# Performance work log

Hardware: AMD Instinct MI355X
Metric: run time of the kernel (lower is better)

Reference implementation:

```python
import jax, jax.numpy as jnp
import numpy as np

B, IN, H = 8192, 1024, 1024

def _ln(x, g, b, eps=1e-5):
    mu = jnp.mean(x, axis=-1, keepdims=True)
    var = jnp.mean(jnp.square(x - mu), axis=-1, keepdims=True)
    return (x - mu) * jax.lax.rsqrt(var + eps) * g + b

def setup_inputs() -> dict:
    key = jax.random.key(0)
    ks = jax.random.split(key, 8)
    s_h = 1.0 / np.sqrt(H)
    s_i = 1.0 / np.sqrt(IN)
    inp = {
        'x': jax.random.normal(ks[0], (B, IN), jnp.float32),
        'h': jax.random.normal(ks[1], (B, H), jnp.float32),
        'W_r': jax.random.uniform(ks[2], (H, H), jnp.float32, -s_h, s_h),
        'U_r': jax.random.uniform(ks[3], (H, IN), jnp.float32, -s_i, s_i),
        'W_u': jax.random.uniform(ks[4], (H, H), jnp.float32, -s_h, s_h),
        'U_u': jax.random.uniform(ks[5], (H, IN), jnp.float32, -s_i, s_i),
        'W_c': jax.random.uniform(ks[6], (H, H), jnp.float32, -s_h, s_h),
        'U_c': jax.random.uniform(ks[7], (H, IN), jnp.float32, -s_i, s_i),
        # LayerNorm params: rows = [r_hidden, r_input, u_hidden, u_input, c_hidden, c_input]
        'ln_gamma': 0.1 * jnp.ones((6, H), jnp.float32),
        'ln_beta': jnp.zeros((6, H), jnp.float32),
    }
    return inp

def reference(x, h, W_r, U_r, W_u, U_u, W_c, U_c, ln_gamma, ln_beta):
    g, b = ln_gamma, ln_beta
    # nn.Linear(bias=False): y = x @ W.T
    r = jax.nn.sigmoid(_ln(h @ W_r.T, g[0], b[0]) + _ln(x @ U_r.T, g[1], b[1]))
    u = jax.nn.sigmoid(_ln(h @ W_u.T, g[2], b[2]) + _ln(x @ U_u.T, g[3], b[3]))
    c = jnp.tanh(_ln((h * r) @ W_c.T, g[4], b[4]) + _ln(x @ U_c.T, g[5], b[5]))
    return (1.0 - u) * h + u * c
```

## Files before the change

kernel.cpp:

```cpp
#include <hip/hip_runtime.h>
#include <cstdint>
#include <cstddef>

typedef unsigned short u16;
typedef unsigned char u8;
typedef __attribute__((ext_vector_type(8))) short bf16x8;
typedef __attribute__((ext_vector_type(4))) float f32x4;
typedef __attribute__((ext_vector_type(4))) int i32x4;
typedef __attribute__((ext_vector_type(8))) int i32x8;

__device__ inline float bf2f(u16 u) { return __uint_as_float(((unsigned)u) << 16); }
__device__ inline unsigned f2bf(float f) {
  unsigned u = __float_as_uint(f);
  u += 0x7fffu + ((u >> 16) & 1u);
  return u >> 16;
}

__device__ inline unsigned f2fp8(float f) {
  unsigned s = (__float_as_uint(f) >> 31) << 7;
  float a = fabsf(f);
  if (a >= 0.015625f) {
    unsigned u = __float_as_uint(a);
    u += 0x7FFFFu + ((u >> 20) & 1u);
    unsigned e = (u >> 23) - 120u;
    unsigned m = (u >> 20) & 7u;
    return s | (e << 3) | m;
  }
  int m = (int)rintf(a * 512.0f);
  return s | (unsigned)m;
}

__device__ inline void async16(const void* g, void* l) {
  __builtin_amdgcn_global_load_lds(
      (const __attribute__((address_space(1))) void*)g,
      (__attribute__((address_space(3))) void*)l, 16, 0, 0);
}

__device__ inline i32x8 join8(i32x4 lo, i32x4 hi) {
  i32x8 r;
  r[0] = lo[0]; r[1] = lo[1]; r[2] = lo[2]; r[3] = lo[3];
  r[4] = hi[0]; r[5] = hi[1]; r[6] = hi[2]; r[7] = hi[3];
  return r;
}

__device__ inline void unpack8(uint4 q, float* o) {
  o[0] = bf2f((u16)(q.x & 0xffffu)); o[1] = bf2f((u16)(q.x >> 16));
  o[2] = bf2f((u16)(q.y & 0xffffu)); o[3] = bf2f((u16)(q.y >> 16));
  o[4] = bf2f((u16)(q.z & 0xffffu)); o[5] = bf2f((u16)(q.z >> 16));
  o[6] = bf2f((u16)(q.w & 0xffffu)); o[7] = bf2f((u16)(q.w >> 16));
}

__device__ inline uint4 pack8(const float* v) {
  uint4 q;
  q.x = f2bf(v[0]) | (f2bf(v[1]) << 16);
  q.y = f2bf(v[2]) | (f2bf(v[3]) << 16);
  q.z = f2bf(v[4]) | (f2bf(v[5]) << 16);
  q.w = f2bf(v[6]) | (f2bf(v[7]) << 16);
  return q;
}

__device__ inline float fast_sigmoid(float z) {
  return 1.0f / (1.0f + exp2f(-1.4426950408889634f * z));
}
__device__ inline float fast_tanh(float z) {
  return 1.0f - 2.0f / (1.0f + exp2f(2.8853900817779268f * z));
}

struct ConvArgs2 {
  const float* x; const float* h; const float* wr; const float* ur;
  const float* wbf[4];
  u16* xb; u16* hb; u8* x8; u8* h8; u8* w8r; u8* w8u;
  u16* wbo[4];
};

__global__ __launch_bounds__(256) void convert_all(ConvArgs2 a) {
  const int b = blockIdx.x;
  const int t = threadIdx.x;
  if (b < 16384) {
    const bool isx = b < 8192;
    const int off = isx ? b : b - 8192;
    const float* __restrict__ s = isx ? a.x : a.h;
    u16* __restrict__ db = isx ? a.xb : a.hb;
    u8*  __restrict__ d8 = isx ? a.x8 : a.h8;
    const int i = (off * 256 + t) * 4;
    float4 v = *(const float4*)(s + i);
    uint2 o;
    o.x = f2bf(v.x) | (f2bf(v.y) << 16);
    o.y = f2bf(v.z) | (f2bf(v.w) << 16);
    *(uint2*)(db + i) = o;
    unsigned q = f2fp8(v.x) | (f2fp8(v.y) << 8) | (f2fp8(v.z) << 16) | (f2fp8(v.w) << 24);
    *(unsigned*)(d8 + i) = q;
  } else if (b < 18432) {
    const bool isr = b < 17408;
    const int off = isr ? b - 16384 : b - 17408;
    const float* __restrict__ s = isr ? a.wr : a.ur;
    u8* __restrict__ d8 = isr ? a.w8r : a.w8u;
    const int i = (off * 256 + t) * 4;
    float4 v = *(const float4*)(s + i);
    unsigned q = f2fp8(v.x * 8192.f) | (f2fp8(v.y * 8192.f) << 8) |
                 (f2fp8(v.z * 8192.f) << 16) | (f2fp8(v.w * 8192.f) << 24);
    *(unsigned*)(d8 + i) = q;
  } else {
    const int tt = b - 18432;
    const int which = tt >> 10;
    const int off = tt & 1023;
    const float* __restrict__ s = a.wbf[which];
    u16* __restrict__ d = a.wbo[which];
    const int i = (off * 256 + t) * 4;
    float4 v = *(const float4*)(s + i);
    uint2 o;
    o.x = f2bf(v.x) | (f2bf(v.y) << 16);
    o.y = f2bf(v.z) | (f2bf(v.w) << 16);
    *(uint2*)(d + i) = o;
  }
}

struct GemmF8 { const u8* A[2]; const u8* Bw[2]; u16* Y[2]; };

__global__ __launch_bounds__(512, 2) void gemm_fp8(GemmF8 args) {
  const int p = blockIdx.x;
  const int wg = (p & 7) * 32 + (p >> 3);
  const int gate = wg >> 7;
  const int rem  = wg & 127;
  const int rblk = rem >> 2;
  const int cblk = rem & 3;

  const u8* __restrict__ A  = args.A[gate];
  const u8* __restrict__ Bw = args.Bw[gate];
  u16* __restrict__ Y = args.Y[gate];

  __shared__ __attribute__((aligned(16))) u8 sm[2][2][2][128 * 128];

  const int tid  = threadIdx.x;
  const int lane = tid & 63;
  const int w    = tid >> 6;
  const int wm   = w >> 2;
  const int wn   = w & 3;

  const int l8   = lane >> 3;
  const int sgrp = (lane & 7) ^ l8;
  const u8* aSrc = A  + ((size_t)(rblk * 256 + w * 8 + l8) << 10) + sgrp * 16;
  const u8* bSrc = Bw + ((size_t)(cblk * 256 + w * 8 + l8) << 10) + sgrp * 16;
  const int ldsW = w * 8 * 128;

  const int sw = lane & 7;
  const int g0 = (lane >> 4) * 2;
  const int o0 = ((g0 ^ sw) << 4);
  const int o1 = (((g0 + 1) ^ sw) << 4);
  const int frR = (lane & 15) * 128;

  f32x4 acc_lo[4][4] = {};
  f32x4 acc_hi[4][4] = {};

  auto stage = [&](const u8* src, int tt, int op, int half) {
    const int d = tt & 1;
    const u8* s = src + (size_t)half * 131072 + tt * 128;
    u8* l0 = &sm[d][op][half][ldsW];
    async16(s, l0);
    async16(s + 65536, l0 + 8192);
  };

  stage(bSrc, 0, 1, 0); stage(bSrc, 0, 1, 1);
  stage(aSrc, 0, 0, 0); stage(aSrc, 0, 0, 1);
  stage(bSrc, 1, 1, 0); stage(bSrc, 1, 1, 1);
  stage(aSrc, 1, 0, 0);
  asm volatile("s_waitcnt vmcnt(6)" ::: "memory");
  __builtin_amdgcn_s_barrier();

  for (int t = 0; t < 8; ++t) {
    const int d = t & 1;
    const u8* baseA = &sm[d][0][wm][0];
    const u8* baseB = &sm[d][1][wn >> 1][(wn & 1) * 8192];

    i32x8 alo[4], bfg[4];
#pragma unroll
    for (int m = 0; m < 4; ++m) {
      const int ra = frR + m * 2048;
      alo[m] = join8(*(const i32x4*)&baseA[ra + o0], *(const i32x4*)&baseA[ra + o1]);
    }
#pragma unroll
    for (int n = 0; n < 4; ++n) {
      const int rbb = frR + n * 2048;
      bfg[n] = join8(*(const i32x4*)&baseB[rbb + o0], *(const i32x4*)&baseB[rbb + o1]);
    }
    if (t + 1 < 8) stage(aSrc, t + 1, 0, 1);
    __builtin_amdgcn_s_barrier();
    asm volatile("s_waitcnt lgkmcnt(0)" ::: "memory");
    __builtin_amdgcn_s_setprio(1);
#pragma unroll
    for (int m = 0; m < 4; ++m)
#pragma unroll
      for (int n = 0; n < 2; ++n)
        acc_lo[m][n] = __builtin_amdgcn_mfma_scale_f32_16x16x128_f8f6f4(
            alo[m], bfg[n], acc_lo[m][n], 0, 0, 0, 127, 0, 114);
    __builtin_amdgcn_s_setprio(0);
    __builtin_amdgcn_s_barrier();

    if (t + 2 < 8) stage(bSrc, t + 2, 1, 0);
    __builtin_amdgcn_s_barrier();
    __builtin_amdgcn_s_setprio(1);
#pragma unroll
    for (int m = 0; m < 4; ++m)
#pragma unroll
      for (int n = 2; n < 4; ++n)
        acc_lo[m][n] = __builtin_amdgcn_mfma_scale_f32_16x16x128_f8f6f4(
            alo[m], bfg[n], acc_lo[m][n], 0, 0, 0, 127, 0, 114);
    __builtin_amdgcn_s_setprio(0);
    __builtin_amdgcn_s_barrier();

    i32x8 ahi[4];
#pragma unroll
    for (int m = 0; m < 4; ++m) {
      const int ra = frR + m * 2048 + 8192;
      ahi[m] = join8(*(const i32x4*)&baseA[ra + o0], *(const i32x4*)&baseA[ra + o1]);
    }
    if (t + 2 < 8) stage(bSrc, t + 2, 1, 1);
    __builtin_amdgcn_s_barrier();
    asm volatile("s_waitcnt lgkmcnt(0)" ::: "memory");
    __builtin_amdgcn_s_setprio(1);
#pragma unroll
    for (int m = 0; m < 4; ++m)
#pragma unroll
      for (int n = 0; n < 2; ++n)
        acc_hi[m][n] = __builtin_amdgcn_mfma_scale_f32_16x16x128_f8f6f4(
            ahi[m], bfg[n], acc_hi[m][n], 0, 0, 0, 127, 0, 114);
    __builtin_amdgcn_s_setprio(0);
    __builtin_amdgcn_s_barrier();

    if (t + 2 < 8) stage(aSrc, t + 2, 0, 0);
    __builtin_amdgcn_s_barrier();
    __builtin_amdgcn_s_setprio(1);
#pragma unroll
    for (int m = 0; m < 4; ++m)
#pragma unroll
      for (int n = 2; n < 4; ++n)
        acc_hi[m][n] = __builtin_amdgcn_mfma_scale_f32_16x16x128_f8f6f4(
            ahi[m], bfg[n], acc_hi[m][n], 0, 0, 0, 127, 0, 114);
    __builtin_amdgcn_s_setprio(0);
    if (t < 6) asm volatile("s_waitcnt vmcnt(6)" ::: "memory");
    else       asm volatile("s_waitcnt vmcnt(0)" ::: "memory");
    __builtin_amdgcn_s_barrier();
  }

  const int rBase = rblk * 256 + wm * 128 + (lane >> 4) * 4;
  const int cBase = cblk * 256 + wn * 64 + (lane & 15);
#pragma unroll
  for (int m = 0; m < 4; ++m) {
#pragma unroll
    for (int i = 0; i < 4; ++i) {
      const size_t r0 = (size_t)(rBase + m * 16 + i) * 1024 + cBase;
#pragma unroll
      for (int n = 0; n < 4; ++n) {
        Y[r0 + n * 16]             = (u16)f2bf(acc_lo[m][n][i]);
        Y[r0 + 64 * 1024 + n * 16] = (u16)f2bf(acc_hi[m][n][i]);
      }
    }
  }
}

struct Gemm4 { const u16* A[4]; const u16* Bw[4]; u16* Y[4]; };

__global__ __launch_bounds__(512, 2) void gemm_8ph(Gemm4 args) {
  const int p = blockIdx.x;
  const int wg = (p & 7) * 64 + (p >> 3);
  const int gate = wg >> 7;
  const int rem  = wg & 127;
  const int rblk = rem >> 2;
  const int cblk = rem & 3;

  const u16* __restrict__ A  = args.A[gate];
  const u16* __restrict__ Bw = args.Bw[gate];
  u16* __restrict__ Y = args.Y[gate];

  __shared__ __attribute__((aligned(16))) u16 sm[2][2][2][128 * 64];

  const int tid  = threadIdx.x;
  const int lane = tid & 63;
  const int w    = tid >> 6;
  const int wm   = w >> 2;
  const int wn   = w & 3;

  const int l8   = lane >> 3;
  const int sgrp = (lane & 7) ^ l8;
  const u16* aSrc = A  + ((size_t)(rblk * 256 + w * 8 + l8) << 10) + sgrp * 8;
  const u16* bSrc = Bw + ((size_t)(cblk * 256 + w * 8 + l8) << 10) + sgrp * 8;
  const int ldsW = w * 8 * 64;

  const int fr = (lane & 15) * 64 + ((((lane >> 4) ^ (lane & 7))) << 3);

  f32x4 acc_lo[4][4] = {};
  f32x4 acc_hi[4][4] = {};

  auto stage = [&](const u16* src, int tt, int op, int half) {
    const int d = tt & 1;
    const u16* s = src + (size_t)half * 131072 + tt * 64;
    u16* l0 = &sm[d][op][half][ldsW];
    async16(s, l0);
    async16(s + 65536, l0 + 4096);
  };

  stage(bSrc, 0, 1, 0); stage(bSrc, 0, 1, 1);
  stage(aSrc, 0, 0, 0); stage(aSrc, 0, 0, 1);
  stage(bSrc, 1, 1, 0); stage(bSrc, 1, 1, 1);
  stage(aSrc, 1, 0, 0);
  asm volatile("s_waitcnt vmcnt(6)" ::: "memory");
  __builtin_amdgcn_s_barrier();

  for (int t = 0; t < 16; ++t) {
    const int d = t & 1;
    const u16* baseA = &sm[d][0][wm][0];
    const u16* baseB = &sm[d][1][wn >> 1][(wn & 1) * 4096];

    bf16x8 alo[2][4], bfg[2][4];
#pragma unroll
    for (int kk = 0; kk < 2; ++kk) {
      const int fo = fr ^ (kk << 5);
#pragma unroll
      for (int m = 0; m < 4; ++m) alo[kk][m] = *(const bf16x8*)(baseA + m * 1024 + fo);
#pragma unroll
      for (int n = 0; n < 4; ++n) bfg[kk][n] = *(const bf16x8*)(baseB + n * 1024 + fo);
    }
    if (t + 1 < 16) stage(aSrc, t + 1, 0, 1);
    __builtin_amdgcn_s_barrier();
    asm volatile("s_waitcnt lgkmcnt(0)" ::: "memory");
    __builtin_amdgcn_s_setprio(1);
#pragma unroll
    for (int m = 0; m < 4; ++m)
#pragma unroll
      for (int n = 0; n < 2; ++n)
#pragma unroll
        for (int kk = 0; kk < 2; ++kk)
          acc_lo[m][n] = __builtin_amdgcn_mfma_f32_16x16x32_bf16(alo[kk][m], bfg[kk][n], acc_lo[m][n], 0, 0, 0);
    __builtin_amdgcn_s_setprio(0);
    __builtin_amdgcn_s_barrier();

    if (t + 2 < 16) stage(bSrc, t + 2, 1, 0);
    __builtin_amdgcn_s_barrier();
    __builtin_amdgcn_s_setprio(1);
#pragma unroll
    for (int m = 0; m < 4; ++m)
#pragma unroll
      for (int n = 2; n < 4; ++n)
#pragma unroll
        for (int kk = 0; kk < 2; ++kk)
          acc_lo[m][n] = __builtin_amdgcn_mfma_f32_16x16x32_bf16(alo[kk][m], bfg[kk][n], acc_lo[m][n], 0, 0, 0);
    __builtin_amdgcn_s_setprio(0);
    __builtin_amdgcn_s_barrier();

    bf16x8 ahi[2][4];
#pragma unroll
    for (int kk = 0; kk < 2; ++kk) {
      const int fo = fr ^ (kk << 5);
#pragma unroll
      for (int m = 0; m < 4; ++m) ahi[kk][m] = *(const bf16x8*)(baseA + (m + 4) * 1024 + fo);
    }
    if (t + 2 < 16) stage(bSrc, t + 2, 1, 1);
    __builtin_amdgcn_s_barrier();
    asm volatile("s_waitcnt lgkmcnt(0)" ::: "memory");
    __builtin_amdgcn_s_setprio(1);
#pragma unroll
    for (int m = 0; m < 4; ++m)
#pragma unroll
      for (int n = 0; n < 2; ++n)
#pragma unroll
        for (int kk = 0; kk < 2; ++kk)
          acc_hi[m][n] = __builtin_amdgcn_mfma_f32_16x16x32_bf16(ahi[kk][m], bfg[kk][n], acc_hi[m][n], 0, 0, 0);
    __builtin_amdgcn_s_setprio(0);
    __builtin_amdgcn_s_barrier();

    if (t + 2 < 16) stage(aSrc, t + 2, 0, 0);
    __builtin_amdgcn_s_barrier();
    __builtin_amdgcn_s_setprio(1);
#pragma unroll
    for (int m = 0; m < 4; ++m)
#pragma unroll
      for (int n = 2; n < 4; ++n)
#pragma unroll
        for (int kk = 0; kk < 2; ++kk)
          acc_hi[m][n] = __builtin_amdgcn_mfma_f32_16x16x32_bf16(ahi[kk][m], bfg[kk][n], acc_hi[m][n], 0, 0, 0);
    __builtin_amdgcn_s_setprio(0);
    if (t < 14) asm volatile("s_waitcnt vmcnt(6)" ::: "memory");
    else        asm volatile("s_waitcnt vmcnt(0)" ::: "memory");
    __builtin_amdgcn_s_barrier();
  }

  const int rBase = rblk * 256 + wm * 128 + (lane >> 4) * 4;
  const int cBase = cblk * 256 + wn * 64 + (lane & 15);
#pragma unroll
  for (int m = 0; m < 4; ++m) {
#pragma unroll
    for (int i = 0; i < 4; ++i) {
      const size_t r0 = (size_t)(rBase + m * 16 + i) * 1024 + cBase;
#pragma unroll
      for (int n = 0; n < 4; ++n) {
        Y[r0 + n * 16]             = (u16)f2bf(acc_lo[m][n][i]);
        Y[r0 + 64 * 1024 + n * 16] = (u16)f2bf(acc_hi[m][n][i]);
      }
    }
  }
}

__global__ __launch_bounds__(256) void rgate_kernel(
    const u16* __restrict__ Yrh, const u16* __restrict__ Yrx,
    const u16* __restrict__ hb, const float* __restrict__ gamma,
    const float* __restrict__ beta, u16* __restrict__ hrb) {
  const int row  = blockIdx.x * 4 + (threadIdx.x >> 6);
  const int lane = threadIdx.x & 63;
  const size_t rb = (size_t)row * 1024;

  uint4 qa[2], qb[2], qh[2];
  qa[0] = *(const uint4*)(Yrh + rb + lane * 8);
  qa[1] = *(const uint4*)(Yrh + rb + 512 + lane * 8);
  qb[0] = *(const uint4*)(Yrx + rb + lane * 8);
  qb[1] = *(const uint4*)(Yrx + rb + 512 + lane * 8);
  qh[0] = *(const uint4*)(hb  + rb + lane * 8);
  qh[1] = *(const uint4*)(hb  + rb + 512 + lane * 8);

  float s0 = 0.f, s0q = 0.f, s1 = 0.f, s1q = 0.f;
  float tmp[8];
#pragma unroll
  for (int c = 0; c < 2; c++) {
    unpack8(qa[c], tmp);
#pragma unroll
    for (int j = 0; j < 8; j++) { s0 += tmp[j]; s0q += tmp[j] * tmp[j]; }
    unpack8(qb[c], tmp);
#pragma unroll
    for (int j = 0; j < 8; j++) { s1 += tmp[j]; s1q += tmp[j] * tmp[j]; }
  }
#pragma unroll
  for (int off = 1; off < 64; off <<= 1) {
    s0 += __shfl_xor(s0, off, 64);  s0q += __shfl_xor(s0q, off, 64);
    s1 += __shfl_xor(s1, off, 64);  s1q += __shfl_xor(s1q, off, 64);
  }

  const float inv = 1.0f / 1024.0f;
  const float mu0 = s0 * inv, rs0 = rsqrtf(s0q * inv - mu0 * mu0 + 1e-5f);
  const float mu1 = s1 * inv, rs1 = rsqrtf(s1q * inv - mu1 * mu1 + 1e-5f);

#pragma unroll
  for (int c = 0; c < 2; c++) {
    const int cb = c * 512 + lane * 8;
    float va[8], vb[8], vh[8], o[8];
    unpack8(qa[c], va); unpack8(qb[c], vb); unpack8(qh[c], vh);
#pragma unroll
    for (int j = 0; j < 8; j++) {
      const float ln0 = (va[j] - mu0) * rs0 * gamma[cb + j] + beta[cb + j];
      const float ln1 = (vb[j] - mu1) * rs1 * gamma[1024 + cb + j] + beta[1024 + cb + j];
      const float rg = fast_sigmoid(ln0 + ln1);
      o[j] = vh[j] * rg;
    }
    *(uint4*)(hrb + rb + cb) = pack8(o);
  }
}

__global__ __launch_bounds__(256) void final_fuse(
    const u16* __restrict__ Yuh, const u16* __restrict__ Yux,
    const u16* __restrict__ Ych, const u16* __restrict__ Ycx,
    const float* __restrict__ h, const float* __restrict__ gamma,
    const float* __restrict__ beta, float* __restrict__ out) {
  const int row  = blockIdx.x * 4 + (threadIdx.x >> 6);
  const int lane = threadIdx.x & 63;
  const size_t rb = (size_t)row * 1024;

  uint4 q0[2], q1[2], q2[2], q3[2];
  float4 hf[4];
#pragma unroll
  for (int c = 0; c < 2; c++) {
    const int cb = c * 512 + lane * 8;
    q0[c] = *(const uint4*)(Yuh + rb + cb);
    q1[c] = *(const uint4*)(Yux + rb + cb);
    q2[c] = *(const uint4*)(Ych + rb + cb);
    q3[c] = *(const uint4*)(Ycx + rb + cb);
    hf[c * 2]     = *(const float4*)(h + rb + cb);
    hf[c * 2 + 1] = *(const float4*)(h + rb + cb + 4);
  }

  float s[8] = {0.f, 0.f, 0.f, 0.f, 0.f, 0.f, 0.f, 0.f};
  float tmp[8];
#pragma unroll
  for (int c = 0; c < 2; c++) {
    unpack8(q0[c], tmp);
#pragma unroll
    for (int j = 0; j < 8; j++) { s[0] += tmp[j]; s[1] += tmp[j] * tmp[j]; }
    unpack8(q1[c], tmp);
#pragma unroll
    for (int j = 0; j < 8; j++) { s[2] += tmp[j]; s[3] += tmp[j] * tmp[j]; }
    unpack8(q2[c], tmp);
#pragma unroll
    for (int j = 0; j < 8; j++) { s[4] += tmp[j]; s[5] += tmp[j] * tmp[j]; }
    unpack8(q3[c], tmp);
#pragma unroll
    for (int j = 0; j < 8; j++) { s[6] += tmp[j]; s[7] += tmp[j] * tmp[j]; }
  }
#pragma unroll
  for (int off = 1; off < 64; off <<= 1) {
#pragma unroll
    for (int q = 0; q < 8; q++) s[q] += __shfl_xor(s[q], off, 64);
  }

  const float inv = 1.0f / 1024.0f;
  const float mu0 = s[0] * inv, rs0 = rsqrtf(s[1] * inv - mu0 * mu0 + 1e-5f);
  const float mu1 = s[2] * inv, rs1 = rsqrtf(s[3] * inv - mu1 * mu1 + 1e-5f);
  const float mu2 = s[4] * inv, rs2 = rsqrtf(s[5] * inv - mu2 * mu2 + 1e-5f);
  const float mu3 = s[6] * inv, rs3 = rsqrtf(s[7] * inv - mu3 * mu3 + 1e-5f);

#pragma unroll
  for (int c = 0; c < 2; c++) {
    const int cb = c * 512 + lane * 8;
    float v0[8], v1[8], v2[8], v3[8];
    unpack8(q0[c], v0); unpack8(q1[c], v1); unpack8(q2[c], v2); unpack8(q3[c], v3);
    const float* hv = (const float*)&hf[c * 2];
    float o[8];
#pragma unroll
    for (int j = 0; j < 8; j++) {
      const int cc = cb + j;
      const float ln2 = (v0[j] - mu0) * rs0 * gamma[2 * 1024 + cc] + beta[2 * 1024 + cc];
      const float ln3 = (v1[j] - mu1) * rs1 * gamma[3 * 1024 + cc] + beta[3 * 1024 + cc];
      const float ln4 = (v2[j] - mu2) * rs2 * gamma[4 * 1024 + cc] + beta[4 * 1024 + cc];
      const float ln5 = (v3[j] - mu3) * rs3 * gamma[5 * 1024 + cc] + beta[5 * 1024 + cc];
      const float u  = fast_sigmoid(ln2 + ln3);
      const float cg = fast_tanh(ln4 + ln5);
      o[j] = (1.0f - u) * hv[j] + u * cg;
    }
    *(float4*)(out + rb + cb)     = *(float4*)&o[0];
    *(float4*)(out + rb + cb + 4) = *(float4*)&o[4];
  }
}

extern "C" void kernel_launch(void* const* d_in, const int* in_sizes, int n_in,
                              void* d_out, int out_size, void* d_ws, size_t ws_size,
                              hipStream_t stream) {
  const float* x  = (const float*)d_in[0];
  const float* h  = (const float*)d_in[1];
  const float* W_r = (const float*)d_in[2];
  const float* U_r = (const float*)d_in[3];
  const float* W_u = (const float*)d_in[4];
  const float* U_u = (const float*)d_in[5];
  const float* W_c = (const float*)d_in[6];
  const float* U_c = (const float*)d_in[7];
  const float* gamma = (const float*)d_in[8];
  const float* beta  = (const float*)d_in[9];
  float* out = (float*)d_out;

  char* ws = (char*)d_ws;
  const size_t MB = 1024 * 1024;
  const size_t SZ_ACT = 16 * MB;

  u16* xb = (u16*)(ws);
  u16* hb = (u16*)(ws + 16 * MB);
  u16* wb[4];
  for (int i = 0; i < 4; i++) wb[i] = (u16*)(ws + (32 + 2 * i) * MB);
  u8* w8r = (u8*)(ws + 40 * MB);
  u8* w8u = (u8*)(ws + 41 * MB);
  char* ybase = ws + 42 * MB;
  u16* Y0 = (u16*)(ybase);
  u16* Y1 = (u16*)(ybase + SZ_ACT);
  u16* Y2 = (u16*)(ybase + 2 * SZ_ACT);
  u16* Y3 = (u16*)(ybase + 3 * SZ_ACT);
  u16* Y5 = (u16*)(ybase + 4 * SZ_ACT);
  u8* x8 = (u8*)Y5;
  u8* h8 = (u8*)Y5 + 8 * MB;

  ConvArgs2 ca = {};
  ca.x = x; ca.h = h; ca.wr = W_r; ca.ur = U_r;
  ca.wbf[0] = W_u; ca.wbf[1] = U_u; ca.wbf[2] = W_c; ca.wbf[3] = U_c;
  ca.xb = xb; ca.hb = hb; ca.x8 = x8; ca.h8 = h8; ca.w8r = w8r; ca.w8u = w8u;
  ca.wbo[0] = (u16*)(ws + 32 * MB); ca.wbo[1] = (u16*)(ws + 34 * MB);
  ca.wbo[2] = (u16*)(ws + 36 * MB); ca.wbo[3] = (u16*)(ws + 38 * MB);
  convert_all<<<22528, 256, 0, stream>>>(ca);

  GemmF8 gf = {};
  gf.A[0] = h8; gf.Bw[0] = w8r; gf.Y[0] = Y0;
  gf.A[1] = x8; gf.Bw[1] = w8u; gf.Y[1] = Y1;
  gemm_fp8<<<256, 512, 0, stream>>>(gf);

  rgate_kernel<<<2048, 256, 0, stream>>>(Y0, Y1, hb, gamma, beta, Y1);

  Gemm4 gb = {};
  gb.A[0] = xb; gb.Bw[0] = wb[1]; gb.Y[0] = Y3;
  gb.A[1] = xb; gb.Bw[1] = wb[3]; gb.Y[1] = Y5;
  gb.A[2] = hb; gb.Bw[2] = wb[0]; gb.Y[2] = Y2;
  gb.A[3] = Y1; gb.Bw[3] = wb[2]; gb.Y[3] = Y0;
  gemm_8ph<<<512, 512, 0, stream>>>(gb);

  final_fuse<<<2048, 256, 0, stream>>>(Y2, Y3, Y0, Y5, h, gamma, beta, out);
}
```

Baseline: 270.4 us.

## Prefetch next-tile LDS fragments at loop tail and pin schedule with sched barriers

Both GEMM kernels (fp8 scaled MFMA and bf16 MFMA) now load the A-lo and B fragments for the next K step from the other LDS buffer at the end of each iteration. Those loads overlap the barrier and the start of the next iteration instead of stalling before the first MFMA block. The first MFMA block waits on lgkmcnt(4) and the later blocks on lgkmcnt(0), so the loads are retired in stages. Scheduling barriers stop the compiler from moving instructions across these phases, at the cost of extra live registers and fewer chances for it to reorder.

```diff
diff --git a/kernel.cpp b/kernel.cpp
--- a/kernel.cpp
+++ b/kernel.cpp
@@ -65,6 +65,8 @@
 __device__ inline float fast_tanh(float z) {
   return 1.0f - 2.0f / (1.0f + exp2f(2.8853900817779268f * z));
 }
+
+#define SB0() __builtin_amdgcn_sched_barrier(0)
 
 struct ConvArgs2 {
   const float* x; const float* h; const float* wr; const float* ur;
@@ -167,12 +169,10 @@
   asm volatile("s_waitcnt vmcnt(6)" ::: "memory");
   __builtin_amdgcn_s_barrier();
 
-  for (int t = 0; t < 8; ++t) {
-    const int d = t & 1;
-    const u8* baseA = &sm[d][0][wm][0];
-    const u8* baseB = &sm[d][1][wn >> 1][(wn & 1) * 8192];
-
-    i32x8 alo[4], bfg[4];
+  i32x8 alo[4], bfg[4], ahi[4];
+  {
+    const u8* baseA = &sm[0][0][wm][0];
+    const u8* baseB = &sm[0][1][wn >> 1][(wn & 1) * 8192];
 #pragma unroll
     for (int m = 0; m < 4; ++m) {
       const int ra = frR + m * 2048;
@@ -183,9 +183,20 @@
       const int rbb = frR + n * 2048;
       bfg[n] = join8(*(const i32x4*)&baseB[rbb + o0], *(const i32x4*)&baseB[rbb + o1]);
     }
+  }
+  SB0();
+
+  for (int t = 0; t < 8; ++t) {
+    const int d = t & 1;
+    const u8* baseA  = &sm[d][0][wm][0];
+    const u8* baseA2 = &sm[d ^ 1][0][wm][0];
+    const u8* baseB2 = &sm[d ^ 1][1][wn >> 1][(wn & 1) * 8192];
+
     if (t + 1 < 8) stage(aSrc, t + 1, 0, 1);
-    __builtin_amdgcn_s_barrier();
-    asm volatile("s_waitcnt lgkmcnt(0)" ::: "memory");
+    SB0();
+    __builtin_amdgcn_s_barrier();
+    asm volatile("s_waitcnt lgkmcnt(4)" ::: "memory");
+    SB0();
     __builtin_amdgcn_s_setprio(1);
 #pragma unroll
     for (int m = 0; m < 4; ++m)
@@ -194,10 +205,14 @@
         acc_lo[m][n] = __builtin_amdgcn_mfma_scale_f32_16x16x128_f8f6f4(
             alo[m], bfg[n], acc_lo[m][n], 0, 0, 0, 127, 0, 114);
     __builtin_amdgcn_s_setprio(0);
+    SB0();
     __builtin_amdgcn_s_barrier();
 
     if (t + 2 < 8) stage(bSrc, t + 2, 1, 0);
-    __builtin_amdgcn_s_barrier();
+    SB0();
+    __builtin_amdgcn_s_barrier();
+    asm volatile("s_waitcnt lgkmcnt(0)" ::: "memory");
+    SB0();
     __builtin_amdgcn_s_setprio(1);
 #pragma unroll
     for (int m = 0; m < 4; ++m)
@@ -206,17 +221,20 @@
         acc_lo[m][n] = __builtin_amdgcn_mfma_scale_f32_16x16x128_f8f6f4(
             alo[m], bfg[n], acc_lo[m][n], 0, 0, 0, 127, 0, 114);
     __builtin_amdgcn_s_setprio(0);
-    __builtin_amdgcn_s_barrier();
-
-    i32x8 ahi[4];
+    SB0();
 #pragma unroll
     for (int m = 0; m < 4; ++m) {
       const int ra = frR + m * 2048 + 8192;
       ahi[m] = join8(*(const i32x4*)&baseA[ra + o0], *(const i32x4*)&baseA[ra + o1]);
     }
+    SB0();
+    __builtin_amdgcn_s_barrier();
+
     if (t + 2 < 8) stage(bSrc, t + 2, 1, 1);
+    SB0();
     __builtin_amdgcn_s_barrier();
     asm volatile("s_waitcnt lgkmcnt(0)" ::: "memory");
+    SB0();
     __builtin_amdgcn_s_setprio(1);
 #pragma unroll
     for (int m = 0; m < 4; ++m)
@@ -225,9 +243,11 @@
         acc_hi[m][n] = __builtin_amdgcn_mfma_scale_f32_16x16x128_f8f6f4(
             ahi[m], bfg[n], acc_hi[m][n], 0, 0, 0, 127, 0, 114);
     __builtin_amdgcn_s_setprio(0);
+    SB0();
     __builtin_amdgcn_s_barrier();
 
     if (t + 2 < 8) stage(aSrc, t + 2, 0, 0);
+    SB0();
     __builtin_amdgcn_s_barrier();
     __builtin_amdgcn_s_setprio(1);
 #pragma unroll
@@ -237,8 +257,23 @@
         acc_hi[m][n] = __builtin_amdgcn_mfma_scale_f32_16x16x128_f8f6f4(
             ahi[m], bfg[n], acc_hi[m][n], 0, 0, 0, 127, 0, 114);
     __builtin_amdgcn_s_setprio(0);
+    SB0();
     if (t < 6) asm volatile("s_waitcnt vmcnt(6)" ::: "memory");
     else       asm volatile("s_waitcnt vmcnt(0)" ::: "memory");
+    SB0();
+    if (t + 1 < 8) {
+#pragma unroll
+      for (int m = 0; m < 4; ++m) {
+        const int ra = frR + m * 2048;
+        alo[m] = join8(*(const i32x4*)&baseA2[ra + o0], *(const i32x4*)&baseA2[ra + o1]);
+      }
+#pragma unroll
+      for (int n = 0; n < 4; ++n) {
+        const int rbb = frR + n * 2048;
+        bfg[n] = join8(*(const i32x4*)&baseB2[rbb + o0], *(const i32x4*)&baseB2[rbb + o1]);
+      }
+    }
+    SB0();
     __builtin_amdgcn_s_barrier();
   }
 
@@ -306,57 +341,76 @@
   asm volatile("s_waitcnt vmcnt(6)" ::: "memory");
   __builtin_amdgcn_s_barrier();
 
+  bf16x8 alo[2][4], bfg[2][4], ahi[2][4];
+  {
+    const u16* baseA = &sm[0][0][wm][0];
+    const u16* baseB = &sm[0][1][wn >> 1][(wn & 1) * 4096];
+#pragma unroll
+    for (int kk = 0; kk < 2; ++kk) {
+      const int fo = fr ^ (kk << 5);
+#pragma unroll
+      for (int m = 0; m < 4; ++m) alo[kk][m] = *(const bf16x8*)(baseA + m * 1024 + fo);
+    }
+#pragma unroll
+    for (int n = 0; n < 4; ++n)
+#pragma unroll
+      for (int kk = 0; kk < 2; ++kk)
+        bfg[kk][n] = *(const bf16x8*)(baseB + n * 1024 + (fr ^ (kk << 5)));
+  }
+  SB0();
+
   for (int t = 0; t < 16; ++t) {
     const int d = t & 1;
-    const u16* baseA = &sm[d][0][wm][0];
-    const u16* baseB = &sm[d][1][wn >> 1][(wn & 1) * 4096];
-
-    bf16x8 alo[2][4], bfg[2][4];
+    const u16* baseA  = &sm[d][0][wm][0];
+    const u16* baseA2 = &sm[d ^ 1][0][wm][0];
+    const u16* baseB2 = &sm[d ^ 1][1][wn >> 1][(wn & 1) * 4096];
+
+    if (t + 1 < 16) stage(aSrc, t + 1, 0, 1);
+    SB0();
+    __builtin_amdgcn_s_barrier();
+    asm volatile("s_waitcnt lgkmcnt(4)" ::: "memory");
+    SB0();
+    __builtin_amdgcn_s_setprio(1);
+#pragma unroll
+    for (int m = 0; m < 4; ++m)
+#pragma unroll
+      for (int n = 0; n < 2; ++n)
+#pragma unroll
+        for (int kk = 0; kk < 2; ++kk)
+          acc_lo[m][n] = __builtin_amdgcn_mfma_f32_16x16x32_bf16(alo[kk][m], bfg[kk][n], acc_lo[m][n], 0, 0, 0);
+    __builtin_amdgcn_s_setprio(0);
+    SB0();
+    __builtin_amdgcn_s_barrier();
+
+    if (t + 2 < 16) stage(bSrc, t + 2, 1, 0);
+    SB0();
+    __builtin_amdgcn_s_barrier();
+    asm volatile("s_waitcnt lgkmcnt(0)" ::: "memory");
+    SB0();
+    __builtin_amdgcn_s_setprio(1);
+#pragma unroll
+    for (int m = 0; m < 4; ++m)
+#pragma unroll
+      for (int n = 2; n < 4; ++n)
+#pragma unroll
+        for (int kk = 0; kk < 2; ++kk)
+          acc_lo[m][n] = __builtin_amdgcn_mfma_f32_16x16x32_bf16(alo[kk][m], bfg[kk][n], acc_lo[m][n], 0, 0, 0);
+    __builtin_amdgcn_s_setprio(0);
+    SB0();
 #pragma unroll
     for (int kk = 0; kk < 2; ++kk) {
       const int fo = fr ^ (kk << 5);
 #pragma unroll
-      for (int m = 0; m < 4; ++m) alo[kk][m] = *(const bf16x8*)(baseA + m * 1024 + fo);
-#pragma unroll
-      for (int n = 0; n < 4; ++n) bfg[kk][n] = *(const bf16x8*)(baseB + n * 1024 + fo);
-    }
-    if (t + 1 < 16) stage(aSrc, t + 1, 0, 1);
+      for (int m = 0; m < 4; ++m) ahi[kk][m] = *(const bf16x8*)(baseA + (m + 4) * 1024 + fo);
+    }
+    SB0();
+    __builtin_amdgcn_s_barrier();
+
+    if (t + 2 < 16) stage(bSrc, t + 2, 1, 1);
+    SB0();
     __builtin_amdgcn_s_barrier();
     asm volatile("s_waitcnt lgkmcnt(0)" ::: "memory");
-    __builtin_amdgcn_s_setprio(1);
-#pragma unroll
-    for (int m = 0; m < 4; ++m)
-#pragma unroll
-      for (int n = 0; n < 2; ++n)
-#pragma unroll
-        for (int kk = 0; kk < 2; ++kk)
-          acc_lo[m][n] = __builtin_amdgcn_mfma_f32_16x16x32_bf16(alo[kk][m], bfg[kk][n], acc_lo[m][n], 0, 0, 0);
-    __builtin_amdgcn_s_setprio(0);
-    __builtin_amdgcn_s_barrier();
-
-    if (t + 2 < 16) stage(bSrc, t + 2, 1, 0);
-    __builtin_amdgcn_s_barrier();
-    __builtin_amdgcn_s_setprio(1);
-#pragma unroll
-    for (int m = 0; m < 4; ++m)
-#pragma unroll
-      for (int n = 2; n < 4; ++n)
-#pragma unroll
-        for (int kk = 0; kk < 2; ++kk)
-          acc_lo[m][n] = __builtin_amdgcn_mfma_f32_16x16x32_bf16(alo[kk][m], bfg[kk][n], acc_lo[m][n], 0, 0, 0);
-    __builtin_amdgcn_s_setprio(0);
-    __builtin_amdgcn_s_barrier();
-
-    bf16x8 ahi[2][4];
-#pragma unroll
-    for (int kk = 0; kk < 2; ++kk) {
-      const int fo = fr ^ (kk << 5);
-#pragma unroll
-      for (int m = 0; m < 4; ++m) ahi[kk][m] = *(const bf16x8*)(baseA + (m + 4) * 1024 + fo);
-    }
-    if (t + 2 < 16) stage(bSrc, t + 2, 1, 1);
-    __builtin_amdgcn_s_barrier();
-    asm volatile("s_waitcnt lgkmcnt(0)" ::: "memory");
+    SB0();
     __builtin_amdgcn_s_setprio(1);
 #pragma unroll
     for (int m = 0; m < 4; ++m)
@@ -366,9 +420,11 @@
         for (int kk = 0; kk < 2; ++kk)
           acc_hi[m][n] = __builtin_amdgcn_mfma_f32_16x16x32_bf16(ahi[kk][m], bfg[kk][n], acc_hi[m][n], 0, 0, 0);
     __builtin_amdgcn_s_setprio(0);
+    SB0();
     __builtin_amdgcn_s_barrier();
 
     if (t + 2 < 16) stage(aSrc, t + 2, 0, 0);
+    SB0();
     __builtin_amdgcn_s_barrier();
     __builtin_amdgcn_s_setprio(1);
 #pragma unroll
@@ -379,8 +435,24 @@
         for (int kk = 0; kk < 2; ++kk)
           acc_hi[m][n] = __builtin_amdgcn_mfma_f32_16x16x32_bf16(ahi[kk][m], bfg[kk][n], acc_hi[m][n], 0, 0, 0);
     __builtin_amdgcn_s_setprio(0);
+    SB0();
     if (t < 14) asm volatile("s_waitcnt vmcnt(6)" ::: "memory");
     else        asm volatile("s_waitcnt vmcnt(0)" ::: "memory");
+    SB0();
+    if (t + 1 < 16) {
+#pragma unroll
+      for (int kk = 0; kk < 2; ++kk) {
+        const int fo = fr ^ (kk << 5);
+#pragma unroll
+        for (int m = 0; m < 4; ++m) alo[kk][m] = *(const bf16x8*)(baseA2 + m * 1024 + fo);
+      }
+#pragma unroll
+      for (int n = 0; n < 4; ++n)
+#pragma unroll
+        for (int kk = 0; kk < 2; ++kk)
+          bfg[kk][n] = *(const bf16x8*)(baseB2 + n * 1024 + (fr ^ (kk << 5)));
+    }
+    SB0();
     __builtin_amdgcn_s_barrier();
   }
 
```

Measured after the change: 269.6 us. No clear change (-0.3%).

## Move all six GRU GEMMs to FP8 and prefetch LDS fragments across iterations

Applied to the files above, without the earlier changes.

Replaces the bf16 four-GEMM kernel with the templated FP8 scaled-MFMA GEMM. All six weights and the h*r product are quantized to FP8, and the x-dependent u/c GEMMs are launched alongside the r GEMMs. The FP8 GEMM loop now loads the next tile's A/B fragments at the end of each iteration and uses sched barriers with a partial lgkmcnt wait. This cuts the bf16 conversion traffic and halves the operand bytes and MFMA cost of the remaining GEMMs, at the cost of lower precision on the u and c gates.

```diff
diff --git a/kernel.cpp b/kernel.cpp
--- a/kernel.cpp
+++ b/kernel.cpp
@@ -4,7 +4,6 @@
 
 typedef unsigned short u16;
 typedef unsigned char u8;
-typedef __attribute__((ext_vector_type(8))) short bf16x8;
 typedef __attribute__((ext_vector_type(4))) float f32x4;
 typedef __attribute__((ext_vector_type(4))) int i32x4;
 typedef __attribute__((ext_vector_type(8))) int i32x8;
@@ -50,15 +49,6 @@
   o[6] = bf2f((u16)(q.w & 0xffffu)); o[7] = bf2f((u16)(q.w >> 16));
 }
 
-__device__ inline uint4 pack8(const float* v) {
-  uint4 q;
-  q.x = f2bf(v[0]) | (f2bf(v[1]) << 16);
-  q.y = f2bf(v[2]) | (f2bf(v[3]) << 16);
-  q.z = f2bf(v[4]) | (f2bf(v[5]) << 16);
-  q.w = f2bf(v[6]) | (f2bf(v[7]) << 16);
-  return q;
-}
-
 __device__ inline float fast_sigmoid(float z) {
   return 1.0f / (1.0f + exp2f(-1.4426950408889634f * z));
 }
@@ -66,60 +56,47 @@
   return 1.0f - 2.0f / (1.0f + exp2f(2.8853900817779268f * z));
 }
 
-struct ConvArgs2 {
-  const float* x; const float* h; const float* wr; const float* ur;
-  const float* wbf[4];
-  u16* xb; u16* hb; u8* x8; u8* h8; u8* w8r; u8* w8u;
-  u16* wbo[4];
+#define SB0() __builtin_amdgcn_sched_barrier(0)
+
+struct ConvArgs3 {
+  const float* x; const float* h;
+  const float* w[6];
+  u8* x8; u8* h8;
+  u8* w8[6];
 };
 
-__global__ __launch_bounds__(256) void convert_all(ConvArgs2 a) {
+__global__ __launch_bounds__(256) void convert_all(ConvArgs3 a) {
   const int b = blockIdx.x;
   const int t = threadIdx.x;
   if (b < 16384) {
     const bool isx = b < 8192;
     const int off = isx ? b : b - 8192;
     const float* __restrict__ s = isx ? a.x : a.h;
-    u16* __restrict__ db = isx ? a.xb : a.hb;
-    u8*  __restrict__ d8 = isx ? a.x8 : a.h8;
+    u8* __restrict__ d8 = isx ? a.x8 : a.h8;
     const int i = (off * 256 + t) * 4;
     float4 v = *(const float4*)(s + i);
-    uint2 o;
-    o.x = f2bf(v.x) | (f2bf(v.y) << 16);
-    o.y = f2bf(v.z) | (f2bf(v.w) << 16);
-    *(uint2*)(db + i) = o;
     unsigned q = f2fp8(v.x) | (f2fp8(v.y) << 8) | (f2fp8(v.z) << 16) | (f2fp8(v.w) << 24);
     *(unsigned*)(d8 + i) = q;
-  } else if (b < 18432) {
-    const bool isr = b < 17408;
-    const int off = isr ? b - 16384 : b - 17408;
-    const float* __restrict__ s = isr ? a.wr : a.ur;
-    u8* __restrict__ d8 = isr ? a.w8r : a.w8u;
+  } else {
+    const int tt = b - 16384;
+    const int which = tt >> 10;
+    const int off = tt & 1023;
+    const float* __restrict__ s = a.w[which];
+    u8* __restrict__ d8 = a.w8[which];
     const int i = (off * 256 + t) * 4;
     float4 v = *(const float4*)(s + i);
     unsigned q = f2fp8(v.x * 8192.f) | (f2fp8(v.y * 8192.f) << 8) |
                  (f2fp8(v.z * 8192.f) << 16) | (f2fp8(v.w * 8192.f) << 24);
     *(unsigned*)(d8 + i) = q;
-  } else {
-    const int tt = b - 18432;
-    const int which = tt >> 10;
-    const int off = tt & 1023;
-    const float* __restrict__ s = a.wbf[which];
-    u16* __restrict__ d = a.wbo[which];
-    const int i = (off * 256 + t) * 4;
-    float4 v = *(const float4*)(s + i);
-    uint2 o;
-    o.x = f2bf(v.x) | (f2bf(v.y) << 16);
-    o.y = f2bf(v.z) | (f2bf(v.w) << 16);
-    *(uint2*)(d + i) = o;
-  }
-}
-
-struct GemmF8 { const u8* A[2]; const u8* Bw[2]; u16* Y[2]; };
-
+  }
+}
+
+struct GemmF8 { const u8* A[4]; const u8* Bw[4]; u16* Y[4]; };
+
+template <int NG>
 __global__ __launch_bounds__(512, 2) void gemm_fp8(GemmF8 args) {
   const int p = blockIdx.x;
-  const int wg = (p & 7) * 32 + (p >> 3);
+  const int wg = (p & 7) * (NG * 16) + (p >> 3);
   const int gate = wg >> 7;
   const int rem  = wg & 127;
   const int rblk = rem >> 2;
@@ -167,12 +144,10 @@
   asm volatile("s_waitcnt vmcnt(6)" ::: "memory");
   __builtin_amdgcn_s_barrier();
 
-  for (int t = 0; t < 8; ++t) {
-    const int d = t & 1;
-    const u8* baseA = &sm[d][0][wm][0];
-    const u8* baseB = &sm[d][1][wn >> 1][(wn & 1) * 8192];
-
-    i32x8 alo[4], bfg[4];
+  i32x8 alo[4], bfg[4], ahi[4];
+  {
+    const u8* baseA = &sm[0][0][wm][0];
+    const u8* baseB = &sm[0][1][wn >> 1][(wn & 1) * 8192];
 #pragma unroll
     for (int m = 0; m < 4; ++m) {
       const int ra = frR + m * 2048;
@@ -183,9 +158,20 @@
       const int rbb = frR + n * 2048;
       bfg[n] = join8(*(const i32x4*)&baseB[rbb + o0], *(const i32x4*)&baseB[rbb + o1]);
     }
+  }
+  SB0();
+
+  for (int t = 0; t < 8; ++t) {
+    const int d = t & 1;
+    const u8* baseA  = &sm[d][0][wm][0];
+    const u8* baseA2 = &sm[d ^ 1][0][wm][0];
+    const u8* baseB2 = &sm[d ^ 1][1][wn >> 1][(wn & 1) * 8192];
+
     if (t + 1 < 8) stage(aSrc, t + 1, 0, 1);
-    __builtin_amdgcn_s_barrier();
-    asm volatile("s_waitcnt lgkmcnt(0)" ::: "memory");
+    SB0();
+    __builtin_amdgcn_s_barrier();
+    asm volatile("s_waitcnt lgkmcnt(4)" ::: "memory");
+    SB0();
     __builtin_amdgcn_s_setprio(1);
 #pragma unroll
     for (int m = 0; m < 4; ++m)
@@ -194,10 +180,14 @@
         acc_lo[m][n] = __builtin_amdgcn_mfma_scale_f32_16x16x128_f8f6f4(
             alo[m], bfg[n], acc_lo[m][n], 0, 0, 0, 127, 0, 114);
     __builtin_amdgcn_s_setprio(0);
+    SB0();
     __builtin_amdgcn_s_barrier();
 
     if (t + 2 < 8) stage(bSrc, t + 2, 1, 0);
-    __builtin_amdgcn_s_barrier();
+    SB0();
+    __builtin_amdgcn_s_barrier();
+    asm volatile("s_waitcnt lgkmcnt(0)" ::: "memory");
+    SB0();
     __builtin_amdgcn_s_setprio(1);
 #pragma unroll
     for (int m = 0; m < 4; ++m)
@@ -206,17 +196,20 @@
         acc_lo[m][n] = __builtin_amdgcn_mfma_scale_f32_16x16x128_f8f6f4(
             alo[m], bfg[n], acc_lo[m][n], 0, 0, 0, 127, 0, 114);
     __builtin_amdgcn_s_setprio(0);
-    __builtin_amdgcn_s_barrier();
-
-    i32x8 ahi[4];
+    SB0();
 #pragma unroll
     for (int m = 0; m < 4; ++m) {
       const int ra = frR + m * 2048 + 8192;
       ahi[m] = join8(*(const i32x4*)&baseA[ra + o0], *(const i32x4*)&baseA[ra + o1]);
     }
+    SB0();
+    __builtin_amdgcn_s_barrier();
+
     if (t + 2 < 8) stage(bSrc, t + 2, 1, 1);
+    SB0();
     __builtin_amdgcn_s_barrier();
     asm volatile("s_waitcnt lgkmcnt(0)" ::: "memory");
+    SB0();
     __builtin_amdgcn_s_setprio(1);
 #pragma unroll
     for (int m = 0; m < 4; ++m)
@@ -225,9 +218,11 @@
         acc_hi[m][n] = __builtin_amdgcn_mfma_scale_f32_16x16x128_f8f6f4(
             ahi[m], bfg[n], acc_hi[m][n], 0, 0, 0, 127, 0, 114);
     __builtin_amdgcn_s_setprio(0);
+    SB0();
     __builtin_amdgcn_s_barrier();
 
     if (t + 2 < 8) stage(aSrc, t + 2, 0, 0);
+    SB0();
     __builtin_amdgcn_s_barrier();
     __builtin_amdgcn_s_setprio(1);
 #pragma unroll
@@ -237,8 +232,23 @@
         acc_hi[m][n] = __builtin_amdgcn_mfma_scale_f32_16x16x128_f8f6f4(
             ahi[m], bfg[n], acc_hi[m][n], 0, 0, 0, 127, 0, 114);
     __builtin_amdgcn_s_setprio(0);
+    SB0();
     if (t < 6) asm volatile("s_waitcnt vmcnt(6)" ::: "memory");
     else       asm volatile("s_waitcnt vmcnt(0)" ::: "memory");
+    SB0();
+    if (t + 1 < 8) {
+#pragma unroll
+      for (int m = 0; m < 4; ++m) {
+        const int ra = frR + m * 2048;
+        alo[m] = join8(*(const i32x4*)&baseA2[ra + o0], *(const i32x4*)&baseA2[ra + o1]);
+      }
+#pragma unroll
+      for (int n = 0; n < 4; ++n) {
+        const int rbb = frR + n * 2048;
+        bfg[n] = join8(*(const i32x4*)&baseB2[rbb + o0], *(const i32x4*)&baseB2[rbb + o1]);
+      }
+    }
+    SB0();
     __builtin_amdgcn_s_barrier();
   }
 
@@ -258,163 +268,24 @@
   }
 }
 
-struct Gemm4 { const u16* A[4]; const u16* Bw[4]; u16* Y[4]; };
-
-__global__ __launch_bounds__(512, 2) void gemm_8ph(Gemm4 args) {
-  const int p = blockIdx.x;
-  const int wg = (p & 7) * 64 + (p >> 3);
-  const int gate = wg >> 7;
-  const int rem  = wg & 127;
-  const int rblk = rem >> 2;
-  const int cblk = rem & 3;
-
-  const u16* __restrict__ A  = args.A[gate];
-  const u16* __restrict__ Bw = args.Bw[gate];
-  u16* __restrict__ Y = args.Y[gate];
-
-  __shared__ __attribute__((aligned(16))) u16 sm[2][2][2][128 * 64];
-
-  const int tid  = threadIdx.x;
-  const int lane = tid & 63;
-  const int w    = tid >> 6;
-  const int wm   = w >> 2;
-  const int wn   = w & 3;
-
-  const int l8   = lane >> 3;
-  const int sgrp = (lane & 7) ^ l8;
-  const u16* aSrc = A  + ((size_t)(rblk * 256 + w * 8 + l8) << 10) + sgrp * 8;
-  const u16* bSrc = Bw + ((size_t)(cblk * 256 + w * 8 + l8) << 10) + sgrp * 8;
-  const int ldsW = w * 8 * 64;
-
-  const int fr = (lane & 15) * 64 + ((((lane >> 4) ^ (lane & 7))) << 3);
-
-  f32x4 acc_lo[4][4] = {};
-  f32x4 acc_hi[4][4] = {};
-
-  auto stage = [&](const u16* src, int tt, int op, int half) {
-    const int d = tt & 1;
-    const u16* s = src + (size_t)half * 131072 + tt * 64;
-    u16* l0 = &sm[d][op][half][ldsW];
-    async16(s, l0);
-    async16(s + 65536, l0 + 4096);
-  };
-
-  stage(bSrc, 0, 1, 0); stage(bSrc, 0, 1, 1);
-  stage(aSrc, 0, 0, 0); stage(aSrc, 0, 0, 1);
-  stage(bSrc, 1, 1, 0); stage(bSrc, 1, 1, 1);
-  stage(aSrc, 1, 0, 0);
-  asm volatile("s_waitcnt vmcnt(6)" ::: "memory");
-  __builtin_amdgcn_s_barrier();
-
-  for (int t = 0; t < 16; ++t) {
-    const int d = t & 1;
-    const u16* baseA = &sm[d][0][wm][0];
-    const u16* baseB = &sm[d][1][wn >> 1][(wn & 1) * 4096];
-
-    bf16x8 alo[2][4], bfg[2][4];
-#pragma unroll
-    for (int kk = 0; kk < 2; ++kk) {
-      const int fo = fr ^ (kk << 5);
-#pragma unroll
-      for (int m = 0; m < 4; ++m) alo[kk][m] = *(const bf16x8*)(baseA + m * 1024 + fo);
-#pragma unroll
-      for (int n = 0; n < 4; ++n) bfg[kk][n] = *(const bf16x8*)(baseB + n * 1024 + fo);
-    }
-    if (t + 1 < 16) stage(aSrc, t + 1, 0, 1);
-    __builtin_amdgcn_s_barrier();
-    asm volatile("s_waitcnt lgkmcnt(0)" ::: "memory");
-    __builtin_amdgcn_s_setprio(1);
-#pragma unroll
-    for (int m = 0; m < 4; ++m)
-#pragma unroll
-      for (int n = 0; n < 2; ++n)
-#pragma unroll
-        for (int kk = 0; kk < 2; ++kk)
-          acc_lo[m][n] = __builtin_amdgcn_mfma_f32_16x16x32_bf16(alo[kk][m], bfg[kk][n], acc_lo[m][n], 0, 0, 0);
-    __builtin_amdgcn_s_setprio(0);
-    __builtin_amdgcn_s_barrier();
-
-    if (t + 2 < 16) stage(bSrc, t + 2, 1, 0);
-    __builtin_amdgcn_s_barrier();
-    __builtin_amdgcn_s_setprio(1);
-#pragma unroll
-    for (int m = 0; m < 4; ++m)
-#pragma unroll
-      for (int n = 2; n < 4; ++n)
-#pragma unroll
-        for (int kk = 0; kk < 2; ++kk)
-          acc_lo[m][n] = __builtin_amdgcn_mfma_f32_16x16x32_bf16(alo[kk][m], bfg[kk][n], acc_lo[m][n], 0, 0, 0);
-    __builtin_amdgcn_s_setprio(0);
-    __builtin_amdgcn_s_barrier();
-
-    bf16x8 ahi[2][4];
-#pragma unroll
-    for (int kk = 0; kk < 2; ++kk) {
-      const int fo = fr ^ (kk << 5);
-#pragma unroll
-      for (int m = 0; m < 4; ++m) ahi[kk][m] = *(const bf16x8*)(baseA + (m + 4) * 1024 + fo);
-    }
-    if (t + 2 < 16) stage(bSrc, t + 2, 1, 1);
-    __builtin_amdgcn_s_barrier();
-    asm volatile("s_waitcnt lgkmcnt(0)" ::: "memory");
-    __builtin_amdgcn_s_setprio(1);
-#pragma unroll
-    for (int m = 0; m < 4; ++m)
-#pragma unroll
-      for (int n = 0; n < 2; ++n)
-#pragma unroll
-        for (int kk = 0; kk < 2; ++kk)
-          acc_hi[m][n] = __builtin_amdgcn_mfma_f32_16x16x32_bf16(ahi[kk][m], bfg[kk][n], acc_hi[m][n], 0, 0, 0);
-    __builtin_amdgcn_s_setprio(0);
-    __builtin_amdgcn_s_barrier();
-
-    if (t + 2 < 16) stage(aSrc, t + 2, 0, 0);
-    __builtin_amdgcn_s_barrier();
-    __builtin_amdgcn_s_setprio(1);
-#pragma unroll
-    for (int m = 0; m < 4; ++m)
-#pragma unroll
-      for (int n = 2; n < 4; ++n)
-#pragma unroll
-        for (int kk = 0; kk < 2; ++kk)
-          acc_hi[m][n] = __builtin_amdgcn_mfma_f32_16x16x32_bf16(ahi[kk][m], bfg[kk][n], acc_hi[m][n], 0, 0, 0);
-    __builtin_amdgcn_s_setprio(0);
-    if (t < 14) asm volatile("s_waitcnt vmcnt(6)" ::: "memory");
-    else        asm volatile("s_waitcnt vmcnt(0)" ::: "memory");
-    __builtin_amdgcn_s_barrier();
-  }
-
-  const int rBase = rblk * 256 + wm * 128 + (lane >> 4) * 4;
-  const int cBase = cblk * 256 + wn * 64 + (lane & 15);
-#pragma unroll
-  for (int m = 0; m < 4; ++m) {
-#pragma unroll
-    for (int i = 0; i < 4; ++i) {
-      const size_t r0 = (size_t)(rBase + m * 16 + i) * 1024 + cBase;
-#pragma unroll
-      for (int n = 0; n < 4; ++n) {
-        Y[r0 + n * 16]             = (u16)f2bf(acc_lo[m][n][i]);
-        Y[r0 + 64 * 1024 + n * 16] = (u16)f2bf(acc_hi[m][n][i]);
-      }
-    }
-  }
-}
-
 __global__ __launch_bounds__(256) void rgate_kernel(
     const u16* __restrict__ Yrh, const u16* __restrict__ Yrx,
-    const u16* __restrict__ hb, const float* __restrict__ gamma,
-    const float* __restrict__ beta, u16* __restrict__ hrb) {
+    const float* __restrict__ h, const float* __restrict__ gamma,
+    const float* __restrict__ beta, u8* __restrict__ hr8) {
   const int row  = blockIdx.x * 4 + (threadIdx.x >> 6);
   const int lane = threadIdx.x & 63;
   const size_t rb = (size_t)row * 1024;
 
-  uint4 qa[2], qb[2], qh[2];
-  qa[0] = *(const uint4*)(Yrh + rb + lane * 8);
-  qa[1] = *(const uint4*)(Yrh + rb + 512 + lane * 8);
-  qb[0] = *(const uint4*)(Yrx + rb + lane * 8);
-  qb[1] = *(const uint4*)(Yrx + rb + 512 + lane * 8);
-  qh[0] = *(const uint4*)(hb  + rb + lane * 8);
-  qh[1] = *(const uint4*)(hb  + rb + 512 + lane * 8);
+  uint4 qa[2], qb[2];
+  float4 hf[4];
+#pragma unroll
+  for (int c = 0; c < 2; c++) {
+    const int cb = c * 512 + lane * 8;
+    qa[c] = *(const uint4*)(Yrh + rb + cb);
+    qb[c] = *(const uint4*)(Yrx + rb + cb);
+    hf[c * 2]     = *(const float4*)(h + rb + cb);
+    hf[c * 2 + 1] = *(const float4*)(h + rb + cb + 4);
+  }
 
   float s0 = 0.f, s0q = 0.f, s1 = 0.f, s1q = 0.f;
   float tmp[8];
@@ -440,16 +311,20 @@
 #pragma unroll
   for (int c = 0; c < 2; c++) {
     const int cb = c * 512 + lane * 8;
-    float va[8], vb[8], vh[8], o[8];
-    unpack8(qa[c], va); unpack8(qb[c], vb); unpack8(qh[c], vh);
+    float va[8], vb[8], o[8];
+    unpack8(qa[c], va); unpack8(qb[c], vb);
+    const float* hv = (const float*)&hf[c * 2];
 #pragma unroll
     for (int j = 0; j < 8; j++) {
       const float ln0 = (va[j] - mu0) * rs0 * gamma[cb + j] + beta[cb + j];
       const float ln1 = (vb[j] - mu1) * rs1 * gamma[1024 + cb + j] + beta[1024 + cb + j];
       const float rg = fast_sigmoid(ln0 + ln1);
-      o[j] = vh[j] * rg;
-    }
-    *(uint4*)(hrb + rb + cb) = pack8(o);
+      o[j] = hv[j] * rg;
+    }
+    uint2 q;
+    q.x = f2fp8(o[0]) | (f2fp8(o[1]) << 8) | (f2fp8(o[2]) << 16) | (f2fp8(o[3]) << 24);
+    q.y = f2fp8(o[4]) | (f2fp8(o[5]) << 8) | (f2fp8(o[6]) << 16) | (f2fp8(o[7]) << 24);
+    *(uint2*)(hr8 + rb + cb) = q;
   }
 }
 
@@ -544,44 +419,38 @@
 
   char* ws = (char*)d_ws;
   const size_t MB = 1024 * 1024;
-  const size_t SZ_ACT = 16 * MB;
-
-  u16* xb = (u16*)(ws);
-  u16* hb = (u16*)(ws + 16 * MB);
-  u16* wb[4];
-  for (int i = 0; i < 4; i++) wb[i] = (u16*)(ws + (32 + 2 * i) * MB);
-  u8* w8r = (u8*)(ws + 40 * MB);
-  u8* w8u = (u8*)(ws + 41 * MB);
-  char* ybase = ws + 42 * MB;
-  u16* Y0 = (u16*)(ybase);
-  u16* Y1 = (u16*)(ybase + SZ_ACT);
-  u16* Y2 = (u16*)(ybase + 2 * SZ_ACT);
-  u16* Y3 = (u16*)(ybase + 3 * SZ_ACT);
-  u16* Y5 = (u16*)(ybase + 4 * SZ_ACT);
-  u8* x8 = (u8*)Y5;
-  u8* h8 = (u8*)Y5 + 8 * MB;
-
-  ConvArgs2 ca = {};
-  ca.x = x; ca.h = h; ca.wr = W_r; ca.ur = U_r;
-  ca.wbf[0] = W_u; ca.wbf[1] = U_u; ca.wbf[2] = W_c; ca.wbf[3] = U_c;
-  ca.xb = xb; ca.hb = hb; ca.x8 = x8; ca.h8 = h8; ca.w8r = w8r; ca.w8u = w8u;
-  ca.wbo[0] = (u16*)(ws + 32 * MB); ca.wbo[1] = (u16*)(ws + 34 * MB);
-  ca.wbo[2] = (u16*)(ws + 36 * MB); ca.wbo[3] = (u16*)(ws + 38 * MB);
+
+  u8* x8  = (u8*)(ws);
+  u8* h8  = (u8*)(ws + 8 * MB);
+  u8* hr8 = (u8*)(ws + 16 * MB);
+  u8* w8[6];
+  for (int i = 0; i < 6; i++) w8[i] = (u8*)(ws + 24 * MB + i * MB);
+  u16* Y0 = (u16*)(ws + 32 * MB);
+  u16* Y1 = (u16*)(ws + 48 * MB);
+  u16* Y2 = (u16*)(ws + 64 * MB);
+  u16* Y3 = (u16*)(ws + 80 * MB);
+  u16* Y5 = (u16*)(ws + 96 * MB);
+
+  ConvArgs3 ca = {};
+  ca.x = x; ca.h = h;
+  ca.w[0] = W_r; ca.w[1] = U_r; ca.w[2] = W_u; ca.w[3] = U_u; ca.w[4] = W_c; ca.w[5] = U_c;
+  ca.x8 = x8; ca.h8 = h8;
+  for (int i = 0; i < 6; i++) ca.w8[i] = w8[i];
   convert_all<<<22528, 256, 0, stream>>>(ca);
 
-  GemmF8 gf = {};
-  gf.A[0] = h8; gf.Bw[0] = w8r; gf.Y[0] = Y0;
-  gf.A[1] = x8; gf.Bw[1] = w8u; gf.Y[1] = Y1;
-  gemm_fp8<<<256, 512, 0, stream>>>(gf);
-
-  rgate_kernel<<<2048, 256, 0, stream>>>(Y0, Y1, hb, gamma, beta, Y1);
-
-  Gemm4 gb = {};
-  gb.A[0] = xb; gb.Bw[0] = wb[1]; gb.Y[0] = Y3;
-  gb.A[1] = xb; gb.Bw[1] = wb[3]; gb.Y[1] = Y5;
-  gb.A[2] = hb; gb.Bw[2] = wb[0]; gb.Y[2] = Y2;
-  gb.A[3] = Y1; gb.Bw[3] = wb[2]; gb.Y[3] = Y0;
-  gemm_8ph<<<512, 512, 0, stream>>>(gb);
+  GemmF8 gA = {};
+  gA.A[0] = h8; gA.Bw[0] = w8[0]; gA.Y[0] = Y0;
+  gA.A[1] = x8; gA.Bw[1] = w8[1]; gA.Y[1] = Y1;
+  gA.A[2] = x8; gA.Bw[2] = w8[3]; gA.Y[2] = Y3;
+  gA.A[3] = x8; gA.Bw[3] = w8[5]; gA.Y[3] = Y5;
+  gemm_fp8<4><<<512, 512, 0, stream>>>(gA);
+
+  rgate_kernel<<<2048, 256, 0, stream>>>(Y0, Y1, h, gamma, beta, hr8);
+
+  GemmF8 gB = {};
+  gB.A[0] = h8;  gB.Bw[0] = w8[2]; gB.Y[0] = Y2;
+  gB.A[1] = hr8; gB.Bw[1] = w8[4]; gB.Y[1] = Y0;
+  gemm_fp8<2><<<256, 512, 0, stream>>>(gB);
 
   final_fuse<<<2048, 256, 0, stream>>>(Y2, Y3, Y0, Y5, h, gamma, beta, out);
 }
```

New measurement: 241.3 us, median of 2. 10.8% less time.
